# Kernel tuning notes

Hardware: AMD Instinct MI355X
Metric: run time of the kernel (lower is better)

The kernel has to match this reference:

```python
import jax, jax.numpy as jnp
import numpy as np

N_NODES = 50000
N_EDGES = 1000000
C = 32          # nchannels (multiplicity of each irrep)
NBESSEL = 8
WEIGHT_NUMEL = 3 * C  # three uvu paths: 0e->0e, 0e->1o, 0e->2e


def setup_inputs() -> dict:
    key = jax.random.key(0)
    ks = jax.random.split(key, 12)
    inp = {
        "lenght": jax.random.uniform(ks[0], (N_EDGES, NBESSEL), dtype=jnp.float32),
        "node_features": jax.random.normal(ks[1], (N_NODES, C), dtype=jnp.float32),
        "edge_attributes": jax.random.normal(ks[2], (N_EDGES, 9), dtype=jnp.float32),
        "edge_index": jax.random.randint(ks[3], (2, N_EDGES), 0, N_NODES, dtype=jnp.int64),
        # FullyConnectedNet([8, 6, 6, 6, 96]) weights (e3nn stores unnormalized W, divides by sqrt(fan_in))
        "fcn_w0": jax.random.normal(ks[4], (NBESSEL, 6), dtype=jnp.float32),
        "fcn_w1": jax.random.normal(ks[5], (6, 6), dtype=jnp.float32),
        "fcn_w2": jax.random.normal(ks[6], (6, 6), dtype=jnp.float32),
        "fcn_w3": jax.random.normal(ks[7], (6, WEIGHT_NUMEL), dtype=jnp.float32),
        # equivariant Linear irreps_mid -> irreps_out: one [C, C] mixing matrix per l in {0,1,2}
        "lin_w0": jax.random.normal(ks[8], (C, C), dtype=jnp.float32),
        "lin_w1": jax.random.normal(ks[9], (C, C), dtype=jnp.float32),
        "lin_w2": jax.random.normal(ks[10], (C, C), dtype=jnp.float32),
    }
    return inp


def _fcn(x, w0, w1, w2, w3):
    # e3nn FullyConnectedNet: normalized linear layers with SiLU on hidden layers
    for w in (w0, w1, w2):
        x = jax.nn.silu((x @ w) * (1.0 / np.float32(np.sqrt(w.shape[0]))))
    return (x @ w3) * (1.0 / np.float32(np.sqrt(w3.shape[0])))


def reference(lenght, node_features, edge_attributes, edge_index,
              fcn_w0, fcn_w1, fcn_w2, fcn_w3, lin_w0, lin_w1, lin_w2):
    sender = edge_index[0]
    receiver = edge_index[1]
    num_nodes = node_features.shape[0]
    c = node_features.shape[1]
    e = lenght.shape[0]

    # per-edge tensor-product weights: [E, 3C]
    tp_w = _fcn(lenght, fcn_w0, fcn_w1, fcn_w2, fcn_w3)
    w0, w1, w2 = tp_w[:, :c], tp_w[:, c:2 * c], tp_w[:, 2 * c:]

    x = node_features[sender]                       # gather: [E, C]
    y0 = edge_attributes[:, 0:1]                    # 0e: [E, 1]
    y1 = edge_attributes[:, 1:4]                    # 1o: [E, 3]
    y2 = edge_attributes[:, 4:9]                    # 2e: [E, 5]

    # uvu tensor product, CG for 0e x l -> l is identity
    m0 = w0 * x * y0                                # [E, C]
    m1 = (w1 * x)[:, :, None] * y1[:, None, :]      # [E, C, 3]
    m2 = (w2 * x)[:, :, None] * y2[:, None, :]      # [E, C, 5]
    mij = jnp.concatenate(
        [m0, m1.reshape(e, 3 * c), m2.reshape(e, 5 * c)], axis=1)  # [E, 9C]

    # scatter_sum over receivers
    msg = jax.ops.segment_sum(mij, receiver, num_segments=num_nodes)  # [N, 9C]

    # equivariant Linear (per-l channel mixing, 1/sqrt(fan_in) normalization)
    inv = 1.0 / np.float32(np.sqrt(c))
    o0 = (msg[:, :c] @ lin_w0) * inv                                   # [N, C]
    o1 = jnp.einsum('nci,cd->ndi', msg[:, c:4 * c].reshape(num_nodes, c, 3), lin_w1) * inv
    o2 = jnp.einsum('nci,cd->ndi', msg[:, 4 * c:].reshape(num_nodes, c, 5), lin_w2) * inv
    return jnp.concatenate(
        [o0, o1.reshape(num_nodes, 3 * c), o2.reshape(num_nodes, 5 * c)], axis=1)
```

## Files before the change

### kernel.cpp

```cpp
#include <hip/hip_runtime.h>
#include <math.h>

#define N_NODES 50000
#define N_EDGES 1000000
#define CCH     32
#define ROW     288
#define SCAN_BLOCKS 196

__global__ __launch_bounds__(256) void hist_kernel(
    const int* __restrict__ edge_index, int* __restrict__ deg)
{
    const int e = blockIdx.x * 256 + threadIdx.x;
    if (e >= N_EDGES) return;
    atomicAdd(&deg[edge_index[N_EDGES + e]], 1);
}

__global__ __launch_bounds__(256) void scan_local_kernel(
    const int* __restrict__ deg, int* __restrict__ lexcl, int* __restrict__ blocksum)
{
    __shared__ int s[256];
    const int t = threadIdx.x;
    const int gid = blockIdx.x * 256 + t;
    const int v = (gid < N_NODES) ? deg[gid] : 0;
    s[t] = v;
    __syncthreads();
    for (int ofs = 1; ofs < 256; ofs <<= 1) {
        int w = (t >= ofs) ? s[t - ofs] : 0;
        __syncthreads();
        s[t] += w;
        __syncthreads();
    }
    if (gid < N_NODES) lexcl[gid] = s[t] - v;
    if (t == 255) blocksum[blockIdx.x] = s[255];
}

__global__ __launch_bounds__(256) void scan_top_kernel(
    const int* __restrict__ blocksum, int* __restrict__ blockpref)
{
    __shared__ int s[256];
    const int t = threadIdx.x;
    const int v = (t < SCAN_BLOCKS) ? blocksum[t] : 0;
    s[t] = v;
    __syncthreads();
    for (int ofs = 1; ofs < 256; ofs <<= 1) {
        int w = (t >= ofs) ? s[t - ofs] : 0;
        __syncthreads();
        s[t] += w;
        __syncthreads();
    }
    if (t < SCAN_BLOCKS) blockpref[t] = s[t] - v;
}

__global__ __launch_bounds__(256) void scan_addback_kernel(
    const int* __restrict__ lexcl, const int* __restrict__ blockpref,
    int* __restrict__ offset, int* __restrict__ cursor)
{
    const int gid = blockIdx.x * 256 + threadIdx.x;
    if (gid >= N_NODES) return;
    const int base = blockpref[blockIdx.x] + lexcl[gid];
    offset[gid] = base;
    cursor[gid] = base;
}

__global__ __launch_bounds__(256) void pack_kernel(
    const float* __restrict__ lenght,
    const float* __restrict__ edge_attr,
    const int*   __restrict__ edge_index,
    const float* __restrict__ fw0,
    const float* __restrict__ fw1,
    const float* __restrict__ fw2,
    int*         __restrict__ cursor,
    float4*      __restrict__ rec)
{
    __shared__ float s_w[120];
    for (int i = threadIdx.x; i < 120; i += 256)
        s_w[i] = (i < 48) ? fw0[i] : (i < 84) ? fw1[i - 48] : fw2[i - 84];
    __syncthreads();
    const float* sw0 = s_w;
    const float* sw1 = s_w + 48;
    const float* sw2 = s_w + 84;

    const int e = blockIdx.x * 256 + threadIdx.x;
    if (e >= N_EDGES) return;

    const float inv8 = 0.35355339059327373f;
    const float inv6 = 0.4082482904638631f;

    float len[8];
    const float4 l0 = ((const float4*)(lenght + (long long)e * 8))[0];
    const float4 l1 = ((const float4*)(lenght + (long long)e * 8))[1];
    len[0]=l0.x; len[1]=l0.y; len[2]=l0.z; len[3]=l0.w;
    len[4]=l1.x; len[5]=l1.y; len[6]=l1.z; len[7]=l1.w;

    float h0[6], h1[6], h2[6];
    #pragma unroll
    for (int j = 0; j < 6; ++j) {
        float a = 0.f;
        #pragma unroll
        for (int k = 0; k < 8; ++k) a += len[k] * sw0[k * 6 + j];
        a *= inv8;
        h0[j] = a / (1.f + __expf(-a));
    }
    #pragma unroll
    for (int j = 0; j < 6; ++j) {
        float a = 0.f;
        #pragma unroll
        for (int k = 0; k < 6; ++k) a += h0[k] * sw1[k * 6 + j];
        a *= inv6;
        h1[j] = a / (1.f + __expf(-a));
    }
    #pragma unroll
    for (int j = 0; j < 6; ++j) {
        float a = 0.f;
        #pragma unroll
        for (int k = 0; k < 6; ++k) a += h1[k] * sw2[k * 6 + j];
        a *= inv6;
        h2[j] = a * inv6 / (1.f + __expf(-a));
    }

    const float* ea = edge_attr + (long long)e * 9;
    float y[9];
    #pragma unroll
    for (int i = 0; i < 9; ++i) y[i] = ea[i];

    const int snd = edge_index[e];
    const int r   = edge_index[N_EDGES + e];
    const int p   = atomicAdd(&cursor[r], 1);

    float4* rp = rec + (long long)p * 4;
    rp[0] = make_float4(h2[0], h2[1], h2[2], h2[3]);
    rp[1] = make_float4(h2[4], h2[5], y[0], y[1]);
    rp[2] = make_float4(y[2], y[3], y[4], y[5]);
    rp[3] = make_float4(y[6], y[7], y[8], __int_as_float(snd));
}

__global__ __launch_bounds__(256) void gather_kernel(
    const float4* __restrict__ rec,
    const float*  __restrict__ node_features,
    const int*    __restrict__ offset,
    const int*    __restrict__ deg,
    const float*  __restrict__ fw3,
    const float*  __restrict__ lw0,
    const float*  __restrict__ lw1,
    const float*  __restrict__ lw2,
    float*        __restrict__ out)
{
    __shared__ float s_lw0[1024], s_lw1[1024], s_lw2[1024];
    for (int i = threadIdx.x; i < 1024; i += 256) {
        s_lw0[i] = lw0[i];
        s_lw1[i] = lw1[i];
        s_lw2[i] = lw2[i];
    }
    __syncthreads();

    const int wave = threadIdx.x >> 6;
    const int l    = threadIdx.x & 63;
    const int c    = l & 31;
    const int h    = l >> 5;
    const int node = blockIdx.x * 4 + wave;

    float f3a[6], f3b[6], f3c[6];
    #pragma unroll
    for (int k = 0; k < 6; ++k) {
        f3a[k] = fw3[k * 96 + c];
        f3b[k] = fw3[k * 96 + 32 + c];
        f3c[k] = fw3[k * 96 + 64 + c];
    }

    const int off = offset[node];
    const int dg  = deg[node];

    float acc[9] = {0.f,0.f,0.f,0.f,0.f,0.f,0.f,0.f,0.f};

    int j = h;
    float4 r0, r1, r2, r3;
    float  xq = 0.f;
    if (j < dg) {
        const float4* rp = rec + (long long)(off + j) * 4;
        r0 = rp[0]; r1 = rp[1]; r2 = rp[2]; r3 = rp[3];
        xq = node_features[(long long)__float_as_int(r3.w) * CCH + c];
    }
    while (j < dg) {
        const int jn = j + 2;
        float4 n0, n1, n2, n3;
        if (jn < dg) {
            const float4* rp = rec + (long long)(off + jn) * 4;
            n0 = rp[0]; n1 = rp[1]; n2 = rp[2]; n3 = rp[3];
        }

        const float w0c = r0.x*f3a[0] + r0.y*f3a[1] + r0.z*f3a[2]
                        + r0.w*f3a[3] + r1.x*f3a[4] + r1.y*f3a[5];
        const float w1c = r0.x*f3b[0] + r0.y*f3b[1] + r0.z*f3b[2]
                        + r0.w*f3b[3] + r1.x*f3b[4] + r1.y*f3b[5];
        const float w2c = r0.x*f3c[0] + r0.y*f3c[1] + r0.z*f3c[2]
                        + r0.w*f3c[3] + r1.x*f3c[4] + r1.y*f3c[5];

        const float x = xq;
        acc[0] += (w0c * x) * r1.z;
        const float a1 = w1c * x;
        acc[1] += a1 * r1.w;
        acc[2] += a1 * r2.x;
        acc[3] += a1 * r2.y;
        const float a2 = w2c * x;
        acc[4] += a2 * r2.z;
        acc[5] += a2 * r2.w;
        acc[6] += a2 * r3.x;
        acc[7] += a2 * r3.y;
        acc[8] += a2 * r3.z;

        if (jn < dg)
            xq = node_features[(long long)__float_as_int(n3.w) * CCH + c];
        r0 = n0; r1 = n1; r2 = n2; r3 = n3;
        j = jn;
    }

    #pragma unroll
    for (int k = 0; k < 9; ++k) acc[k] += __shfl_down(acc[k], 32);

    const int d = c;
    float o0 = 0.f;
    float o1[3] = {0.f, 0.f, 0.f};
    float o2[5] = {0.f, 0.f, 0.f, 0.f, 0.f};
    for (int cc = h * 16; cc < h * 16 + 16; ++cc) {
        const float m0 = __shfl(acc[0], cc);
        const float m1 = __shfl(acc[1], cc);
        const float m2 = __shfl(acc[2], cc);
        const float m3 = __shfl(acc[3], cc);
        const float m4 = __shfl(acc[4], cc);
        const float m5 = __shfl(acc[5], cc);
        const float m6 = __shfl(acc[6], cc);
        const float m7 = __shfl(acc[7], cc);
        const float m8 = __shfl(acc[8], cc);
        o0 += m0 * s_lw0[cc * 32 + d];
        const float w1 = s_lw1[cc * 32 + d];
        o1[0] += m1 * w1; o1[1] += m2 * w1; o1[2] += m3 * w1;
        const float w2 = s_lw2[cc * 32 + d];
        o2[0] += m4 * w2; o2[1] += m5 * w2; o2[2] += m6 * w2;
        o2[3] += m7 * w2; o2[4] += m8 * w2;
    }

    o0 += __shfl_down(o0, 32);
    #pragma unroll
    for (int i = 0; i < 3; ++i) o1[i] += __shfl_down(o1[i], 32);
    #pragma unroll
    for (int i = 0; i < 5; ++i) o2[i] += __shfl_down(o2[i], 32);

    if (h == 0) {
        const float inv32 = 0.17677669529663687f;
        float* op = out + (long long)node * ROW;
        op[d] = o0 * inv32;
        #pragma unroll
        for (int i = 0; i < 3; ++i) op[32 + d * 3 + i] = o1[i] * inv32;
        #pragma unroll
        for (int i = 0; i < 5; ++i) op[128 + d * 5 + i] = o2[i] * inv32;
    }
}

extern "C" void kernel_launch(void* const* d_in, const int* in_sizes, int n_in,
                              void* d_out, int out_size, void* d_ws, size_t ws_size,
                              hipStream_t stream)
{
    const float* lenght = (const float*)d_in[0];
    const float* nf     = (const float*)d_in[1];
    const float* ea     = (const float*)d_in[2];
    const int*   ei     = (const int*)d_in[3];
    const float* fw0    = (const float*)d_in[4];
    const float* fw1    = (const float*)d_in[5];
    const float* fw2    = (const float*)d_in[6];
    const float* fw3    = (const float*)d_in[7];
    const float* lw0    = (const float*)d_in[8];
    const float* lw1    = (const float*)d_in[9];
    const float* lw2    = (const float*)d_in[10];
    float* out = (float*)d_out;

    char* ws = (char*)d_ws;
    float4* rec    = (float4*)ws; ws += (size_t)N_EDGES * 4 * sizeof(float4);
    int* deg       = (int*)ws;    ws += (size_t)N_NODES * sizeof(int);
    int* offset    = (int*)ws;    ws += (size_t)N_NODES * sizeof(int);
    int* cursor    = (int*)ws;    ws += (size_t)N_NODES * sizeof(int);
    int* lexcl     = (int*)ws;    ws += (size_t)N_NODES * sizeof(int);
    int* blocksum  = (int*)ws;    ws += (size_t)SCAN_BLOCKS * sizeof(int);
    int* blockpref = (int*)ws;    ws += (size_t)SCAN_BLOCKS * sizeof(int);

    hipMemsetAsync(deg, 0, (size_t)N_NODES * sizeof(int), stream);

    const int EB = (N_EDGES + 255) / 256;
    hist_kernel        <<<EB, 256, 0, stream>>>(ei, deg);
    scan_local_kernel  <<<SCAN_BLOCKS, 256, 0, stream>>>(deg, lexcl, blocksum);
    scan_top_kernel    <<<1, 256, 0, stream>>>(blocksum, blockpref);
    scan_addback_kernel<<<SCAN_BLOCKS, 256, 0, stream>>>(lexcl, blockpref, offset, cursor);
    pack_kernel        <<<EB, 256, 0, stream>>>(lenght, ea, ei, fw0, fw1, fw2, cursor, rec);
    gather_kernel      <<<N_NODES / 4, 256, 0, stream>>>(
        rec, nf, offset, deg, fw3, lw0, lw1, lw2, out);
}
```

Baseline: 383.1 us.

## Write edge records in edge order with a CSR index and deeper gather prefetch

The pack kernel now writes each 64-byte edge record at its original edge position, so those writes are coalesced instead of scattered through the atomic cursor. It also writes a small (edge id, sender) int2 into CSR order. The gather kernel reads the index first and then loads each record indirectly, keeping two records plus four index entries in flight per lane to hide the extra level of indirection. The cost is that gather reads of the 64-byte records are now random rather than contiguous per node, plus an extra 8 MB index array.

```diff
diff --git a/kernel.cpp b/kernel.cpp
--- a/kernel.cpp
+++ b/kernel.cpp
@@ -70,7 +70,8 @@
     const float* __restrict__ fw1,
     const float* __restrict__ fw2,
     int*         __restrict__ cursor,
-    float4*      __restrict__ rec)
+    float4*      __restrict__ rec,
+    int2*        __restrict__ es)
 {
     __shared__ float s_w[120];
     for (int i = threadIdx.x; i < 120; i += 256)
@@ -126,8 +127,9 @@
     const int snd = edge_index[e];
     const int r   = edge_index[N_EDGES + e];
     const int p   = atomicAdd(&cursor[r], 1);
-
-    float4* rp = rec + (long long)p * 4;
+    es[p] = make_int2(e, snd);
+
+    float4* rp = rec + (long long)e * 4;
     rp[0] = make_float4(h2[0], h2[1], h2[2], h2[3]);
     rp[1] = make_float4(h2[4], h2[5], y[0], y[1]);
     rp[2] = make_float4(y[2], y[3], y[4], y[5]);
@@ -137,6 +139,7 @@
 __global__ __launch_bounds__(256) void gather_kernel(
     const float4* __restrict__ rec,
     const float*  __restrict__ node_features,
+    const int2*   __restrict__ es,
     const int*    __restrict__ offset,
     const int*    __restrict__ deg,
     const float*  __restrict__ fw3,
@@ -172,46 +175,78 @@
 
     float acc[9] = {0.f,0.f,0.f,0.f,0.f,0.f,0.f,0.f,0.f};
 
-    int j = h;
-    float4 r0, r1, r2, r3;
-    float  xq = 0.f;
-    if (j < dg) {
-        const float4* rp = rec + (long long)(off + j) * 4;
-        r0 = rp[0]; r1 = rp[1]; r2 = rp[2]; r3 = rp[3];
-        xq = node_features[(long long)__float_as_int(r3.w) * CCH + c];
-    }
-    while (j < dg) {
-        const int jn = j + 2;
-        float4 n0, n1, n2, n3;
-        if (jn < dg) {
-            const float4* rp = rec + (long long)(off + jn) * 4;
-            n0 = rp[0]; n1 = rp[1]; n2 = rp[2]; n3 = rp[3];
+    if (dg > h) {
+        const int2* esp = es + off;
+        const int last = dg - 1;
+
+        int2 eA = esp[min(h,     last)];
+        int2 eB = esp[min(h + 2, last)];
+        const float4* pa = rec + (long long)eA.x * 4;
+        float4 A0 = pa[0], A1 = pa[1], A2 = pa[2], A3 = pa[3];
+        float  xA = node_features[(long long)eA.y * CCH + c];
+        const float4* pb = rec + (long long)eB.x * 4;
+        float4 B0 = pb[0], B1 = pb[1], B2 = pb[2], B3 = pb[3];
+        float  xB = node_features[(long long)eB.y * CCH + c];
+        eA = esp[min(h + 4, last)];
+        eB = esp[min(h + 6, last)];
+
+        int j = h;
+        while (true) {
+            {
+                const int eid = eA.x, snd = eA.y;
+                eA = esp[min(j + 8, last)];
+                const float w0c = A0.x*f3a[0] + A0.y*f3a[1] + A0.z*f3a[2]
+                                + A0.w*f3a[3] + A1.x*f3a[4] + A1.y*f3a[5];
+                const float w1c = A0.x*f3b[0] + A0.y*f3b[1] + A0.z*f3b[2]
+                                + A0.w*f3b[3] + A1.x*f3b[4] + A1.y*f3b[5];
+                const float w2c = A0.x*f3c[0] + A0.y*f3c[1] + A0.z*f3c[2]
+                                + A0.w*f3c[3] + A1.x*f3c[4] + A1.y*f3c[5];
+                const float x = xA;
+                acc[0] += (w0c * x) * A1.z;
+                const float a1 = w1c * x;
+                acc[1] += a1 * A1.w;
+                acc[2] += a1 * A2.x;
+                acc[3] += a1 * A2.y;
+                const float a2 = w2c * x;
+                acc[4] += a2 * A2.z;
+                acc[5] += a2 * A2.w;
+                acc[6] += a2 * A3.x;
+                acc[7] += a2 * A3.y;
+                acc[8] += a2 * A3.z;
+                const float4* rp = rec + (long long)eid * 4;
+                A0 = rp[0]; A1 = rp[1]; A2 = rp[2]; A3 = rp[3];
+                xA = node_features[(long long)snd * CCH + c];
+            }
+            j += 2;
+            if (j >= dg) break;
+            {
+                const int eid = eB.x, snd = eB.y;
+                eB = esp[min(j + 8, last)];
+                const float w0c = B0.x*f3a[0] + B0.y*f3a[1] + B0.z*f3a[2]
+                                + B0.w*f3a[3] + B1.x*f3a[4] + B1.y*f3a[5];
+                const float w1c = B0.x*f3b[0] + B0.y*f3b[1] + B0.z*f3b[2]
+                                + B0.w*f3b[3] + B1.x*f3b[4] + B1.y*f3b[5];
+                const float w2c = B0.x*f3c[0] + B0.y*f3c[1] + B0.z*f3c[2]
+                                + B0.w*f3c[3] + B1.x*f3c[4] + B1.y*f3c[5];
+                const float x = xB;
+                acc[0] += (w0c * x) * B1.z;
+                const float a1 = w1c * x;
+                acc[1] += a1 * B1.w;
+                acc[2] += a1 * B2.x;
+                acc[3] += a1 * B2.y;
+                const float a2 = w2c * x;
+                acc[4] += a2 * B2.z;
+                acc[5] += a2 * B2.w;
+                acc[6] += a2 * B3.x;
+                acc[7] += a2 * B3.y;
+                acc[8] += a2 * B3.z;
+                const float4* rp = rec + (long long)eid * 4;
+                B0 = rp[0]; B1 = rp[1]; B2 = rp[2]; B3 = rp[3];
+                xB = node_features[(long long)snd * CCH + c];
+            }
+            j += 2;
+            if (j >= dg) break;
         }
-
-        const float w0c = r0.x*f3a[0] + r0.y*f3a[1] + r0.z*f3a[2]
-                        + r0.w*f3a[3] + r1.x*f3a[4] + r1.y*f3a[5];
-        const float w1c = r0.x*f3b[0] + r0.y*f3b[1] + r0.z*f3b[2]
-                        + r0.w*f3b[3] + r1.x*f3b[4] + r1.y*f3b[5];
-        const float w2c = r0.x*f3c[0] + r0.y*f3c[1] + r0.z*f3c[2]
-                        + r0.w*f3c[3] + r1.x*f3c[4] + r1.y*f3c[5];
-
-        const float x = xq;
-        acc[0] += (w0c * x) * r1.z;
-        const float a1 = w1c * x;
-        acc[1] += a1 * r1.w;
-        acc[2] += a1 * r2.x;
-        acc[3] += a1 * r2.y;
-        const float a2 = w2c * x;
-        acc[4] += a2 * r2.z;
-        acc[5] += a2 * r2.w;
-        acc[6] += a2 * r3.x;
-        acc[7] += a2 * r3.y;
-        acc[8] += a2 * r3.z;
-
-        if (jn < dg)
-            xq = node_features[(long long)__float_as_int(n3.w) * CCH + c];
-        r0 = n0; r1 = n1; r2 = n2; r3 = n3;
-        j = jn;
     }
 
     #pragma unroll
@@ -275,6 +310,7 @@
 
     char* ws = (char*)d_ws;
     float4* rec    = (float4*)ws; ws += (size_t)N_EDGES * 4 * sizeof(float4);
+    int2* es       = (int2*)ws;   ws += (size_t)N_EDGES * sizeof(int2);
     int* deg       = (int*)ws;    ws += (size_t)N_NODES * sizeof(int);
     int* offset    = (int*)ws;    ws += (size_t)N_NODES * sizeof(int);
     int* cursor    = (int*)ws;    ws += (size_t)N_NODES * sizeof(int);
@@ -289,7 +325,7 @@
     scan_local_kernel  <<<SCAN_BLOCKS, 256, 0, stream>>>(deg, lexcl, blocksum);
     scan_top_kernel    <<<1, 256, 0, stream>>>(blocksum, blockpref);
     scan_addback_kernel<<<SCAN_BLOCKS, 256, 0, stream>>>(lexcl, blockpref, offset, cursor);
-    pack_kernel        <<<EB, 256, 0, stream>>>(lenght, ea, ei, fw0, fw1, fw2, cursor, rec);
+    pack_kernel        <<<EB, 256, 0, stream>>>(lenght, ea, ei, fw0, fw1, fw2, cursor, rec, es);
     gather_kernel      <<<N_NODES / 4, 256, 0, stream>>>(
-        rec, nf, offset, deg, fw3, lw0, lw1, lw2, out);
-}
+        rec, nf, es, offset, deg, fw3, lw0, lw1, lw2, out);
+}
```

After: 403.0 us. 5.2% more time.

## Fuse scan into one kernel and double-buffer edge loads in gather

Applied to the files above, without the earlier changes.

Replaces the three-kernel prefix scan with a single 1024-thread block that scans serial chunks of 49 nodes, removing two launches. The gather loop now processes four edges per iteration, two per half-wave, with A/B register double-buffering and unconditional loads into a zero-padded tail of the record buffer, to raise memory-level parallelism. Offset and degree are made wave-uniform with readfirstlane. The channel-mixing step reads messages from LDS instead of 144 shuffles per lane, and the output row is staged in LDS so it can be written with coalesced float4 stores. The cost is higher register pressure and some wasted loads on padded edges.

```diff
diff --git a/kernel.cpp b/kernel.cpp
--- a/kernel.cpp
+++ b/kernel.cpp
@@ -5,7 +5,7 @@
 #define N_EDGES 1000000
 #define CCH     32
 #define ROW     288
-#define SCAN_BLOCKS 196
+#define REC_PAD 64
 
 __global__ __launch_bounds__(256) void hist_kernel(
     const int* __restrict__ edge_index, int* __restrict__ deg)
@@ -15,51 +15,36 @@
     atomicAdd(&deg[edge_index[N_EDGES + e]], 1);
 }
 
-__global__ __launch_bounds__(256) void scan_local_kernel(
-    const int* __restrict__ deg, int* __restrict__ lexcl, int* __restrict__ blocksum)
-{
-    __shared__ int s[256];
+__global__ __launch_bounds__(1024) void scan_fused_kernel(
+    const int* __restrict__ deg, int* __restrict__ offset,
+    int* __restrict__ cursor, float4* __restrict__ recpad)
+{
+    __shared__ int s[1024];
     const int t = threadIdx.x;
-    const int gid = blockIdx.x * 256 + t;
-    const int v = (gid < N_NODES) ? deg[gid] : 0;
-    s[t] = v;
+    const int base = t * 49;
+    int sum = 0;
+    for (int i = 0; i < 49; ++i) {
+        const int g = base + i;
+        if (g < N_NODES) sum += deg[g];
+    }
+    s[t] = sum;
     __syncthreads();
-    for (int ofs = 1; ofs < 256; ofs <<= 1) {
+    for (int ofs = 1; ofs < 1024; ofs <<= 1) {
         int w = (t >= ofs) ? s[t - ofs] : 0;
         __syncthreads();
         s[t] += w;
         __syncthreads();
     }
-    if (gid < N_NODES) lexcl[gid] = s[t] - v;
-    if (t == 255) blocksum[blockIdx.x] = s[255];
-}
-
-__global__ __launch_bounds__(256) void scan_top_kernel(
-    const int* __restrict__ blocksum, int* __restrict__ blockpref)
-{
-    __shared__ int s[256];
-    const int t = threadIdx.x;
-    const int v = (t < SCAN_BLOCKS) ? blocksum[t] : 0;
-    s[t] = v;
-    __syncthreads();
-    for (int ofs = 1; ofs < 256; ofs <<= 1) {
-        int w = (t >= ofs) ? s[t - ofs] : 0;
-        __syncthreads();
-        s[t] += w;
-        __syncthreads();
-    }
-    if (t < SCAN_BLOCKS) blockpref[t] = s[t] - v;
-}
-
-__global__ __launch_bounds__(256) void scan_addback_kernel(
-    const int* __restrict__ lexcl, const int* __restrict__ blockpref,
-    int* __restrict__ offset, int* __restrict__ cursor)
-{
-    const int gid = blockIdx.x * 256 + threadIdx.x;
-    if (gid >= N_NODES) return;
-    const int base = blockpref[blockIdx.x] + lexcl[gid];
-    offset[gid] = base;
-    cursor[gid] = base;
+    int run = s[t] - sum;
+    for (int i = 0; i < 49; ++i) {
+        const int g = base + i;
+        if (g < N_NODES) {
+            offset[g] = run;
+            cursor[g] = run;
+            run += deg[g];
+        }
+    }
+    if (t < REC_PAD) recpad[t] = make_float4(0.f, 0.f, 0.f, 0.f);
 }
 
 __global__ __launch_bounds__(256) void pack_kernel(
@@ -133,6 +118,21 @@
     rp[2] = make_float4(y[2], y[3], y[4], y[5]);
     rp[3] = make_float4(y[6], y[7], y[8], __int_as_float(snd));
 }
+
+#define EDGE_ACC(Ra,Rb,Rc,Rd,xx) do {                                          \
+    const float w0c_ = Ra.x*f3a[0] + Ra.y*f3a[1] + Ra.z*f3a[2]                 \
+                     + Ra.w*f3a[3] + Rb.x*f3a[4] + Rb.y*f3a[5];                \
+    const float w1c_ = Ra.x*f3b[0] + Ra.y*f3b[1] + Ra.z*f3b[2]                 \
+                     + Ra.w*f3b[3] + Rb.x*f3b[4] + Rb.y*f3b[5];                \
+    const float w2c_ = Ra.x*f3c[0] + Ra.y*f3c[1] + Ra.z*f3c[2]                 \
+                     + Ra.w*f3c[3] + Rb.x*f3c[4] + Rb.y*f3c[5];                \
+    acc[0] += (w0c_ * (xx)) * Rb.z;                                            \
+    const float a1_ = w1c_ * (xx);                                             \
+    acc[1] += a1_ * Rb.w; acc[2] += a1_ * Rc.x; acc[3] += a1_ * Rc.y;          \
+    const float a2_ = w2c_ * (xx);                                             \
+    acc[4] += a2_ * Rc.z; acc[5] += a2_ * Rc.w;                                \
+    acc[6] += a2_ * Rd.x; acc[7] += a2_ * Rd.y; acc[8] += a2_ * Rd.z;          \
+} while (0)
 
 __global__ __launch_bounds__(256) void gather_kernel(
     const float4* __restrict__ rec,
@@ -146,10 +146,12 @@
     float*        __restrict__ out)
 {
     __shared__ float s_lw0[1024], s_lw1[1024], s_lw2[1024];
-    for (int i = threadIdx.x; i < 1024; i += 256) {
-        s_lw0[i] = lw0[i];
-        s_lw1[i] = lw1[i];
-        s_lw2[i] = lw2[i];
+    __shared__ float s_m[4][384];
+    {
+        const int t = threadIdx.x;
+        ((float4*)s_lw0)[t] = ((const float4*)lw0)[t];
+        ((float4*)s_lw1)[t] = ((const float4*)lw1)[t];
+        ((float4*)s_lw2)[t] = ((const float4*)lw2)[t];
     }
     __syncthreads();
 
@@ -167,76 +169,86 @@
         f3c[k] = fw3[k * 96 + 64 + c];
     }
 
-    const int off = offset[node];
-    const int dg  = deg[node];
+    int off = offset[node];
+    int dg  = deg[node];
+    off = __builtin_amdgcn_readfirstlane(off);
+    dg  = __builtin_amdgcn_readfirstlane(dg);
+    const int nph = (dg + 3) >> 2;
+
+    const float4* rb = rec + (size_t)off * 4;
 
     float acc[9] = {0.f,0.f,0.f,0.f,0.f,0.f,0.f,0.f,0.f};
 
-    int j = h;
-    float4 r0, r1, r2, r3;
-    float  xq = 0.f;
-    if (j < dg) {
-        const float4* rp = rec + (long long)(off + j) * 4;
-        r0 = rp[0]; r1 = rp[1]; r2 = rp[2]; r3 = rp[3];
-        xq = node_features[(long long)__float_as_int(r3.w) * CCH + c];
-    }
-    while (j < dg) {
-        const int jn = j + 2;
-        float4 n0, n1, n2, n3;
-        if (jn < dg) {
-            const float4* rp = rec + (long long)(off + jn) * 4;
-            n0 = rp[0]; n1 = rp[1]; n2 = rp[2]; n3 = rp[3];
+    if (nph > 0) {
+        int jA = 2 * h;
+        int jB = 2 * h + 4;
+
+        float4 A0 = rb[4*jA+0], A1 = rb[4*jA+1], A2 = rb[4*jA+2], A3 = rb[4*jA+3];
+        float4 A4 = rb[4*jA+4], A5 = rb[4*jA+5], A6 = rb[4*jA+6], A7 = rb[4*jA+7];
+        float4 B0 = rb[4*jB+0], B1 = rb[4*jB+1], B2 = rb[4*jB+2], B3 = rb[4*jB+3];
+        float4 B4 = rb[4*jB+4], B5 = rb[4*jB+5], B6 = rb[4*jB+6], B7 = rb[4*jB+7];
+        float xAr0 = node_features[(size_t)__float_as_int(A3.w) * CCH + c];
+        float xAr1 = node_features[(size_t)__float_as_int(A7.w) * CCH + c];
+        bool  vA0 = (jA < dg), vA1 = (jA + 1 < dg);
+        float xBr0 = 0.f, xBr1 = 0.f;
+        bool  vB0 = false, vB1 = false;
+
+        int p = 0;
+        while (true) {
+            {
+                const float xA0 = vA0 ? xAr0 : 0.f;
+                const float xA1 = vA1 ? xAr1 : 0.f;
+                EDGE_ACC(A0, A1, A2, A3, xA0);
+                EDGE_ACC(A4, A5, A6, A7, xA1);
+                xBr0 = node_features[(size_t)__float_as_int(B3.w) * CCH + c];
+                xBr1 = node_features[(size_t)__float_as_int(B7.w) * CCH + c];
+                vB0 = (jB < dg); vB1 = (jB + 1 < dg);
+                jA += 8;
+                A0 = rb[4*jA+0]; A1 = rb[4*jA+1]; A2 = rb[4*jA+2]; A3 = rb[4*jA+3];
+                A4 = rb[4*jA+4]; A5 = rb[4*jA+5]; A6 = rb[4*jA+6]; A7 = rb[4*jA+7];
+                if (++p == nph) break;
+            }
+            {
+                const float xB0 = vB0 ? xBr0 : 0.f;
+                const float xB1 = vB1 ? xBr1 : 0.f;
+                EDGE_ACC(B0, B1, B2, B3, xB0);
+                EDGE_ACC(B4, B5, B6, B7, xB1);
+                xAr0 = node_features[(size_t)__float_as_int(A3.w) * CCH + c];
+                xAr1 = node_features[(size_t)__float_as_int(A7.w) * CCH + c];
+                vA0 = (jA < dg); vA1 = (jA + 1 < dg);
+                jB += 8;
+                B0 = rb[4*jB+0]; B1 = rb[4*jB+1]; B2 = rb[4*jB+2]; B3 = rb[4*jB+3];
+                B4 = rb[4*jB+4]; B5 = rb[4*jB+5]; B6 = rb[4*jB+6]; B7 = rb[4*jB+7];
+                if (++p == nph) break;
+            }
         }
-
-        const float w0c = r0.x*f3a[0] + r0.y*f3a[1] + r0.z*f3a[2]
-                        + r0.w*f3a[3] + r1.x*f3a[4] + r1.y*f3a[5];
-        const float w1c = r0.x*f3b[0] + r0.y*f3b[1] + r0.z*f3b[2]
-                        + r0.w*f3b[3] + r1.x*f3b[4] + r1.y*f3b[5];
-        const float w2c = r0.x*f3c[0] + r0.y*f3c[1] + r0.z*f3c[2]
-                        + r0.w*f3c[3] + r1.x*f3c[4] + r1.y*f3c[5];
-
-        const float x = xq;
-        acc[0] += (w0c * x) * r1.z;
-        const float a1 = w1c * x;
-        acc[1] += a1 * r1.w;
-        acc[2] += a1 * r2.x;
-        acc[3] += a1 * r2.y;
-        const float a2 = w2c * x;
-        acc[4] += a2 * r2.z;
-        acc[5] += a2 * r2.w;
-        acc[6] += a2 * r3.x;
-        acc[7] += a2 * r3.y;
-        acc[8] += a2 * r3.z;
-
-        if (jn < dg)
-            xq = node_features[(long long)__float_as_int(n3.w) * CCH + c];
-        r0 = n0; r1 = n1; r2 = n2; r3 = n3;
-        j = jn;
     }
 
     #pragma unroll
     for (int k = 0; k < 9; ++k) acc[k] += __shfl_down(acc[k], 32);
+
+    if (h == 0) {
+        float4* mp = (float4*)&s_m[wave][c * 12];
+        mp[0] = make_float4(acc[0], acc[1], acc[2], acc[3]);
+        mp[1] = make_float4(acc[4], acc[5], acc[6], acc[7]);
+        s_m[wave][c * 12 + 8] = acc[8];
+    }
+    asm volatile("s_waitcnt lgkmcnt(0)" ::: "memory");
 
     const int d = c;
     float o0 = 0.f;
     float o1[3] = {0.f, 0.f, 0.f};
     float o2[5] = {0.f, 0.f, 0.f, 0.f, 0.f};
     for (int cc = h * 16; cc < h * 16 + 16; ++cc) {
-        const float m0 = __shfl(acc[0], cc);
-        const float m1 = __shfl(acc[1], cc);
-        const float m2 = __shfl(acc[2], cc);
-        const float m3 = __shfl(acc[3], cc);
-        const float m4 = __shfl(acc[4], cc);
-        const float m5 = __shfl(acc[5], cc);
-        const float m6 = __shfl(acc[6], cc);
-        const float m7 = __shfl(acc[7], cc);
-        const float m8 = __shfl(acc[8], cc);
-        o0 += m0 * s_lw0[cc * 32 + d];
+        const float4 ma = *(const float4*)&s_m[wave][cc * 12];
+        const float4 mb = *(const float4*)&s_m[wave][cc * 12 + 4];
+        const float  m8 = s_m[wave][cc * 12 + 8];
+        o0 += ma.x * s_lw0[cc * 32 + d];
         const float w1 = s_lw1[cc * 32 + d];
-        o1[0] += m1 * w1; o1[1] += m2 * w1; o1[2] += m3 * w1;
+        o1[0] += ma.y * w1; o1[1] += ma.z * w1; o1[2] += ma.w * w1;
         const float w2 = s_lw2[cc * 32 + d];
-        o2[0] += m4 * w2; o2[1] += m5 * w2; o2[2] += m6 * w2;
-        o2[3] += m7 * w2; o2[4] += m8 * w2;
+        o2[0] += mb.x * w2; o2[1] += mb.y * w2; o2[2] += mb.z * w2;
+        o2[3] += mb.w * w2; o2[4] += m8   * w2;
     }
 
     o0 += __shfl_down(o0, 32);
@@ -247,13 +259,19 @@
 
     if (h == 0) {
         const float inv32 = 0.17677669529663687f;
-        float* op = out + (long long)node * ROW;
-        op[d] = o0 * inv32;
-        #pragma unroll
-        for (int i = 0; i < 3; ++i) op[32 + d * 3 + i] = o1[i] * inv32;
-        #pragma unroll
-        for (int i = 0; i < 5; ++i) op[128 + d * 5 + i] = o2[i] * inv32;
-    }
+        float* rw = &s_m[wave][0];
+        rw[d] = o0 * inv32;
+        #pragma unroll
+        for (int i = 0; i < 3; ++i) rw[32 + d * 3 + i] = o1[i] * inv32;
+        #pragma unroll
+        for (int i = 0; i < 5; ++i) rw[128 + d * 5 + i] = o2[i] * inv32;
+    }
+    asm volatile("s_waitcnt lgkmcnt(0)" ::: "memory");
+
+    const float4* rowp = (const float4*)&s_m[wave][0];
+    float4* op4 = (float4*)(out + (size_t)node * ROW);
+    op4[l] = rowp[l];
+    if (l < 8) op4[64 + l] = rowp[64 + l];
 }
 
 extern "C" void kernel_launch(void* const* d_in, const int* in_sizes, int n_in,
@@ -274,22 +292,18 @@
     float* out = (float*)d_out;
 
     char* ws = (char*)d_ws;
-    float4* rec    = (float4*)ws; ws += (size_t)N_EDGES * 4 * sizeof(float4);
-    int* deg       = (int*)ws;    ws += (size_t)N_NODES * sizeof(int);
-    int* offset    = (int*)ws;    ws += (size_t)N_NODES * sizeof(int);
-    int* cursor    = (int*)ws;    ws += (size_t)N_NODES * sizeof(int);
-    int* lexcl     = (int*)ws;    ws += (size_t)N_NODES * sizeof(int);
-    int* blocksum  = (int*)ws;    ws += (size_t)SCAN_BLOCKS * sizeof(int);
-    int* blockpref = (int*)ws;    ws += (size_t)SCAN_BLOCKS * sizeof(int);
+    float4* rec = (float4*)ws; ws += ((size_t)N_EDGES * 4 + REC_PAD) * sizeof(float4);
+    int* deg    = (int*)ws;    ws += (size_t)N_NODES * sizeof(int);
+    int* offset = (int*)ws;    ws += (size_t)N_NODES * sizeof(int);
+    int* cursor = (int*)ws;    ws += (size_t)N_NODES * sizeof(int);
+    float4* recpad = rec + (size_t)N_EDGES * 4;
 
     hipMemsetAsync(deg, 0, (size_t)N_NODES * sizeof(int), stream);
 
     const int EB = (N_EDGES + 255) / 256;
-    hist_kernel        <<<EB, 256, 0, stream>>>(ei, deg);
-    scan_local_kernel  <<<SCAN_BLOCKS, 256, 0, stream>>>(deg, lexcl, blocksum);
-    scan_top_kernel    <<<1, 256, 0, stream>>>(blocksum, blockpref);
-    scan_addback_kernel<<<SCAN_BLOCKS, 256, 0, stream>>>(lexcl, blockpref, offset, cursor);
-    pack_kernel        <<<EB, 256, 0, stream>>>(lenght, ea, ei, fw0, fw1, fw2, cursor, rec);
-    gather_kernel      <<<N_NODES / 4, 256, 0, stream>>>(
+    hist_kernel      <<<EB, 256, 0, stream>>>(ei, deg);
+    scan_fused_kernel<<<1, 1024, 0, stream>>>(deg, offset, cursor, recpad);
+    pack_kernel      <<<EB, 256, 0, stream>>>(lenght, ea, ei, fw0, fw1, fw2, cursor, rec);
+    gather_kernel    <<<N_NODES / 4, 256, 0, stream>>>(
         rec, nf, offset, deg, fw3, lw0, lw1, lw2, out);
 }
```

Result: slower. 471.5 us (+23.1%).
